# Performance work log

Measured on AMD Instinct MI355X. Metric: run time of the kernel, lower is better.

Reference implementation:

```python
import jax, jax.numpy as jnp
import numpy as np

N_NODES = 100000
N_EDGES = 1600000
IN_DIM = 128
OUT_DIM = 128


def setup_inputs() -> dict:
    key = jax.random.key(0)
    k_x, k_r, k_c, k_v, k_w, k_b = jax.random.split(key, 6)
    x = jax.random.normal(k_x, (N_NODES, IN_DIM), dtype=jnp.float32)
    rows = jax.random.randint(k_r, (N_EDGES,), 0, N_NODES, dtype=jnp.int32)
    cols = jax.random.randint(k_c, (N_EDGES,), 0, N_NODES, dtype=jnp.int32)
    vals = jax.random.uniform(k_v, (N_EDGES,), dtype=jnp.float32)
    # nn.Linear(in_dim, out_dim): kaiming-uniform-ish init, exact values irrelevant
    bound = 1.0 / np.sqrt(IN_DIM)
    W = jax.random.uniform(k_w, (IN_DIM, OUT_DIM), dtype=jnp.float32, minval=-bound, maxval=bound)
    b = jax.random.uniform(k_b, (OUT_DIM,), dtype=jnp.float32, minval=-bound, maxval=bound)
    return {"x": x, "W": W, "b": b, "vals": vals, "rows": rows, "cols": cols}


def reference(x, W, b, vals, rows, cols):
    # x = self.linear(x)
    h = x @ W + b  # [N, out_dim]
    # x = torch.sparse.mm(adj, x): out[r] += vals[e] * h[cols[e]] for each edge e with rows[e]==r
    msgs = vals[:, None] * h[cols]  # [E, out_dim]
    out = jax.ops.segment_sum(msgs, rows, num_segments=N_NODES)  # [N, out_dim]
    return out
```

## Files before the change

### kernel.cpp

```cpp
#include <hip/hip_runtime.h>

#define N_NODES 100000
#define N_EDGES 1600000
#define DIM 128
#define NBKT 1563
#define B1   256
#define EPB  6250
#define CAP2 1408
#define GEMM_NB 1563

typedef __attribute__((ext_vector_type(8))) short bf16x8;
typedef __attribute__((ext_vector_type(4))) float f32x4;

__device__ __forceinline__ unsigned short f2bf(float f) {
    unsigned u = __float_as_uint(f);
    u += 0x7FFF + ((u >> 16) & 1);
    return (unsigned short)(u >> 16);
}
__device__ __forceinline__ float bflo(unsigned u) { return __uint_as_float(u << 16); }
__device__ __forceinline__ float bfhi(unsigned u) { return __uint_as_float(u & 0xFFFF0000u); }

__global__ __launch_bounds__(256) void wt_pack(const float* __restrict__ W,
                                               uint4* __restrict__ wtf,
                                               int* __restrict__ gcnt) {
    const int t = blockIdx.x * 256 + threadIdx.x;
    if (t < NBKT) gcnt[t] = 0;
    const int f = t >> 6;
    const int l = t & 63;
    const int kc = f >> 3, nt = f & 7;
    const int quad = l >> 4, n = l & 15;
    unsigned o[4];
    #pragma unroll
    for (int jj = 0; jj < 4; ++jj) {
        const int k0 = kc * 32 + quad * 8 + jj * 2;
        const unsigned short lo = f2bf(W[(k0 + 0) * DIM + nt * 16 + n]);
        const unsigned short hi = f2bf(W[(k0 + 1) * DIM + nt * 16 + n]);
        o[jj] = (unsigned)lo | ((unsigned)hi << 16);
    }
    wtf[t] = make_uint4(o[0], o[1], o[2], o[3]);
}

#define ROWSTRIDE 136
__global__ __launch_bounds__(256) void gemm_count(const float* __restrict__ x,
                                                  const uint4* __restrict__ wtf,
                                                  const float* __restrict__ b,
                                                  unsigned short* __restrict__ h,
                                                  const int* __restrict__ rows,
                                                  int* __restrict__ gcnt) {
    __shared__ uint4 smem4[4 * 16 * ROWSTRIDE / 8];
    if (blockIdx.x >= GEMM_NB) {
        int* c = (int*)smem4;
        const int k = blockIdx.x - GEMM_NB, t = threadIdx.x;
        for (int bb = t; bb < NBKT; bb += 256) c[bb] = 0;
        __syncthreads();
        const int e0 = k * EPB;
        #pragma unroll
        for (int i = 0; i < 6; ++i) {
            const int4 r4 = *(const int4*)&rows[e0 + (t + i * 256) * 4];
            atomicAdd(&c[r4.x >> 6], 1);
            atomicAdd(&c[r4.y >> 6], 1);
            atomicAdd(&c[r4.z >> 6], 1);
            atomicAdd(&c[r4.w >> 6], 1);
        }
        if (t < EPB - 6144) atomicAdd(&c[rows[e0 + 6144 + t] >> 6], 1);
        __syncthreads();
        for (int bb = t; bb < NBKT; bb += 256) {
            const int v = c[bb];
            if (v) atomicAdd(&gcnt[bb], v);
        }
        return;
    }

    const int wave = threadIdx.x >> 6;
    const int lane = threadIdx.x & 63;
    const int quad = lane >> 4;
    const int m = lane & 15;
    const int row_base = blockIdx.x * 64 + wave * 16;
    const int row = row_base + m;
    const bool rok = (row < N_NODES);

    uint4 bf[32];
    #pragma unroll
    for (int f = 0; f < 32; ++f) bf[f] = wtf[f * 64 + lane];

    bf16x8 af[4];
    #pragma unroll
    for (int kc = 0; kc < 4; ++kc) {
        float4 v0, v1;
        if (rok) {
            v0 = *(const float4*)&x[(size_t)row * DIM + kc * 32 + quad * 8];
            v1 = *(const float4*)&x[(size_t)row * DIM + kc * 32 + quad * 8 + 4];
        } else {
            v0 = make_float4(0.f, 0.f, 0.f, 0.f);
            v1 = make_float4(0.f, 0.f, 0.f, 0.f);
        }
        union { bf16x8 v; unsigned u[4]; } a;
        a.u[0] = (unsigned)f2bf(v0.x) | ((unsigned)f2bf(v0.y) << 16);
        a.u[1] = (unsigned)f2bf(v0.z) | ((unsigned)f2bf(v0.w) << 16);
        a.u[2] = (unsigned)f2bf(v1.x) | ((unsigned)f2bf(v1.y) << 16);
        a.u[3] = (unsigned)f2bf(v1.z) | ((unsigned)f2bf(v1.w) << 16);
        af[kc] = a.v;
    }

    f32x4 acc[8];
    #pragma unroll
    for (int nt = 0; nt < 8; ++nt) {
        const float bv = b[nt * 16 + m];
        acc[nt] = (f32x4){bv, bv, bv, bv};
    }

    #pragma unroll
    for (int kc = 0; kc < 4; ++kc) {
        #pragma unroll
        for (int nt = 0; nt < 8; ++nt) {
            union { uint4 u; bf16x8 v; } bb; bb.u = bf[kc * 8 + nt];
            acc[nt] = __builtin_amdgcn_mfma_f32_16x16x32_bf16(af[kc], bb.v, acc[nt], 0, 0, 0);
        }
    }

    unsigned short* sh = (unsigned short*)smem4 + wave * 16 * ROWSTRIDE;
    #pragma unroll
    for (int nt = 0; nt < 8; ++nt) {
        #pragma unroll
        for (int i = 0; i < 4; ++i)
            sh[(quad * 4 + i) * ROWSTRIDE + nt * 16 + m] = f2bf(acc[nt][i]);
    }
    __syncthreads();
    uint4* hv4 = (uint4*)h;
    const int seg = lane & 15;
    #pragma unroll
    for (int c = 0; c < 4; ++c) {
        const int rl = (lane >> 4) + c * 4;
        const int r = row_base + rl;
        const uint4 v = *(const uint4*)&sh[rl * ROWSTRIDE + seg * 8];
        if (r < N_NODES) hv4[(size_t)r * 16 + seg] = v;
    }
}

__global__ __launch_bounds__(1024) void p1_scan(const int* __restrict__ gcnt,
                                                int* __restrict__ bktbase,
                                                int* __restrict__ gcur) {
    __shared__ int s[1024];
    const int t = threadIdx.x;
    const int i0 = 2 * t, i1 = 2 * t + 1;
    const int x0 = (i0 < NBKT) ? gcnt[i0] : 0;
    const int x1 = (i1 < NBKT) ? gcnt[i1] : 0;
    s[t] = x0 + x1;
    __syncthreads();
    for (int o = 1; o < 1024; o <<= 1) {
        const int add = (t >= o) ? s[t - o] : 0;
        __syncthreads();
        s[t] += add;
        __syncthreads();
    }
    const int excl = s[t] - x0 - x1;
    if (i0 < NBKT) { bktbase[i0] = excl; gcur[i0] = excl; }
    if (i1 <= NBKT) {
        bktbase[i1] = excl + x0;
        if (i1 < NBKT) gcur[i1] = excl + x0;
    }
}

__global__ __launch_bounds__(256) void p1_scatter(const int* __restrict__ rows,
                                                  const int* __restrict__ cols,
                                                  const float* __restrict__ vals,
                                                  int* __restrict__ gcur,
                                                  int2* __restrict__ binned) {
    __shared__ int c[NBKT];
    __shared__ int cur[NBKT];
    const int k = blockIdx.x, t = threadIdx.x;
    for (int bb = t; bb < NBKT; bb += 256) c[bb] = 0;
    __syncthreads();
    const int e0 = k * EPB;
    #pragma unroll
    for (int i = 0; i < 6; ++i) {
        const int4 r4 = *(const int4*)&rows[e0 + (t + i * 256) * 4];
        atomicAdd(&c[r4.x >> 6], 1);
        atomicAdd(&c[r4.y >> 6], 1);
        atomicAdd(&c[r4.z >> 6], 1);
        atomicAdd(&c[r4.w >> 6], 1);
    }
    if (t < EPB - 6144) atomicAdd(&c[rows[e0 + 6144 + t] >> 6], 1);
    __syncthreads();
    for (int bb = t; bb < NBKT; bb += 256) {
        const int cc = c[bb];
        if (cc) cur[bb] = atomicAdd(&gcur[bb], cc);
    }
    __syncthreads();
    #pragma unroll
    for (int i = 0; i < 6; ++i) {
        const int g = (t + i * 256) * 4;
        const int4   r4 = *(const int4*)&rows[e0 + g];
        const int4   c4 = *(const int4*)&cols[e0 + g];
        const float4 v4 = *(const float4*)&vals[e0 + g];
        int p;
        p = atomicAdd(&cur[r4.x >> 6], 1);
        binned[p] = make_int2(((r4.x & 63) << 24) | c4.x, __float_as_int(v4.x));
        p = atomicAdd(&cur[r4.y >> 6], 1);
        binned[p] = make_int2(((r4.y & 63) << 24) | c4.y, __float_as_int(v4.y));
        p = atomicAdd(&cur[r4.z >> 6], 1);
        binned[p] = make_int2(((r4.z & 63) << 24) | c4.z, __float_as_int(v4.z));
        p = atomicAdd(&cur[r4.w >> 6], 1);
        binned[p] = make_int2(((r4.w & 63) << 24) | c4.w, __float_as_int(v4.w));
    }
    if (t < EPB - 6144) {
        const int e = e0 + 6144 + t;
        const int r = rows[e];
        const int p = atomicAdd(&cur[r >> 6], 1);
        binned[p] = make_int2(((r & 63) << 24) | cols[e], __float_as_int(vals[e]));
    }
}

__global__ __launch_bounds__(256) void p2_gather(const unsigned* __restrict__ h32,
                                                 const int2* __restrict__ binned,
                                                 const int* __restrict__ bktbase,
                                                 float* __restrict__ out) {
    __shared__ int2 ebuf[CAP2];
    __shared__ int rcount[64], rstart[64], rcur[64], sscan[64];
    const int b = blockIdx.x, t = threadIdx.x;
    const int s0 = bktbase[b];
    const int n = bktbase[b + 1] - s0;

    int2 ereg[6];
    int nm = 0;
    #pragma unroll
    for (int jj = 0; jj < 6; ++jj) {
        const int j = t + jj * 256;
        if (j < n) { ereg[jj] = binned[s0 + j]; nm = jj + 1; }
    }

    if (t < 64) rcount[t] = 0;
    __syncthreads();
    #pragma unroll
    for (int jj = 0; jj < 6; ++jj)
        if (jj < nm) atomicAdd(&rcount[((unsigned)ereg[jj].x) >> 24], 1);
    __syncthreads();

    if (t < 64) sscan[t] = rcount[t];
    __syncthreads();
    for (int o = 1; o < 64; o <<= 1) {
        const int add = (t < 64 && t >= o) ? sscan[t - o] : 0;
        __syncthreads();
        if (t < 64) sscan[t] += add;
        __syncthreads();
    }
    if (t < 64) { rstart[t] = sscan[t] - rcount[t]; rcur[t] = sscan[t] - rcount[t]; }
    __syncthreads();

    #pragma unroll
    for (int jj = 0; jj < 6; ++jj)
        if (jj < nm) {
            const int lr = ((unsigned)ereg[jj].x) >> 24;
            const int pos = atomicAdd(&rcur[lr], 1);
            ebuf[pos] = make_int2(ereg[jj].x & 0x00FFFFFF, ereg[jj].y);
        }
    __syncthreads();

    const int wave = t >> 6, lane = t & 63;
    const char* hbase = (const char*)h32;
    const unsigned lane4 = (unsigned)lane * 4u;

    for (int i = 0; i < 8; ++i) {
        const int lr0 = wave * 16 + i;
        const int lr1 = lr0 + 8;
        const int r0 = b * 64 + lr0;
        const int r1 = b * 64 + lr1;
        const int st0 = rstart[lr0], cn0 = rcount[lr0];
        const int st1 = rstart[lr1], cn1 = rcount[lr1];

        float a0x = 0.f, a0y = 0.f, c0x = 0.f, c0y = 0.f;
        float a1x = 0.f, a1y = 0.f, c1x = 0.f, c1y = 0.f;
        int j0 = 0, j1 = 0;

        while (j0 + 2 <= cn0 && j1 + 2 <= cn1) {
            const int2 e0 = ebuf[st0 + j0], e1 = ebuf[st0 + j0 + 1];
            const int2 f0 = ebuf[st1 + j1], f1 = ebuf[st1 + j1 + 1];
            const unsigned u0 = *(const unsigned*)(hbase + ((((unsigned)e0.x) << 8) | lane4));
            const unsigned u1 = *(const unsigned*)(hbase + ((((unsigned)e1.x) << 8) | lane4));
            const unsigned w0 = *(const unsigned*)(hbase + ((((unsigned)f0.x) << 8) | lane4));
            const unsigned w1 = *(const unsigned*)(hbase + ((((unsigned)f1.x) << 8) | lane4));
            const float v0 = __int_as_float(e0.y), v1 = __int_as_float(e1.y);
            const float s0v = __int_as_float(f0.y), s1v = __int_as_float(f1.y);
            a0x = fmaf(v0, bflo(u0), a0x);  a0y = fmaf(v0, bfhi(u0), a0y);
            c0x = fmaf(v1, bflo(u1), c0x);  c0y = fmaf(v1, bfhi(u1), c0y);
            a1x = fmaf(s0v, bflo(w0), a1x); a1y = fmaf(s0v, bfhi(w0), a1y);
            c1x = fmaf(s1v, bflo(w1), c1x); c1y = fmaf(s1v, bfhi(w1), c1y);
            j0 += 2; j1 += 2;
        }
        for (; j0 + 2 <= cn0; j0 += 2) {
            const int2 e0 = ebuf[st0 + j0], e1 = ebuf[st0 + j0 + 1];
            const unsigned u0 = *(const unsigned*)(hbase + ((((unsigned)e0.x) << 8) | lane4));
            const unsigned u1 = *(const unsigned*)(hbase + ((((unsigned)e1.x) << 8) | lane4));
            const float v0 = __int_as_float(e0.y), v1 = __int_as_float(e1.y);
            a0x = fmaf(v0, bflo(u0), a0x); a0y = fmaf(v0, bfhi(u0), a0y);
            c0x = fmaf(v1, bflo(u1), c0x); c0y = fmaf(v1, bfhi(u1), c0y);
        }
        if (j0 < cn0) {
            const int2 e0 = ebuf[st0 + j0];
            const unsigned u0 = *(const unsigned*)(hbase + ((((unsigned)e0.x) << 8) | lane4));
            const float v0 = __int_as_float(e0.y);
            a0x = fmaf(v0, bflo(u0), a0x); a0y = fmaf(v0, bfhi(u0), a0y);
        }
        for (; j1 + 2 <= cn1; j1 += 2) {
            const int2 f0 = ebuf[st1 + j1], f1 = ebuf[st1 + j1 + 1];
            const unsigned w0 = *(const unsigned*)(hbase + ((((unsigned)f0.x) << 8) | lane4));
            const unsigned w1 = *(const unsigned*)(hbase + ((((unsigned)f1.x) << 8) | lane4));
            const float s0v = __int_as_float(f0.y), s1v = __int_as_float(f1.y);
            a1x = fmaf(s0v, bflo(w0), a1x); a1y = fmaf(s0v, bfhi(w0), a1y);
            c1x = fmaf(s1v, bflo(w1), c1x); c1y = fmaf(s1v, bfhi(w1), c1y);
        }
        if (j1 < cn1) {
            const int2 f0 = ebuf[st1 + j1];
            const unsigned w0 = *(const unsigned*)(hbase + ((((unsigned)f0.x) << 8) | lane4));
            const float s0v = __int_as_float(f0.y);
            a1x = fmaf(s0v, bflo(w0), a1x); a1y = fmaf(s0v, bfhi(w0), a1y);
        }

        if (r0 < N_NODES) {
            float2 o; o.x = a0x + c0x; o.y = a0y + c0y;
            *(float2*)&out[(size_t)r0 * DIM + lane * 2] = o;
        }
        if (r1 < N_NODES) {
            float2 o; o.x = a1x + c1x; o.y = a1y + c1y;
            *(float2*)&out[(size_t)r1 * DIM + lane * 2] = o;
        }
    }
}

extern "C" void kernel_launch(void* const* d_in, const int* in_sizes, int n_in,
                              void* d_out, int out_size, void* d_ws, size_t ws_size,
                              hipStream_t stream) {
    const float* x    = (const float*)d_in[0];
    const float* W    = (const float*)d_in[1];
    const float* b    = (const float*)d_in[2];
    const float* vals = (const float*)d_in[3];
    const int*   rows = (const int*)d_in[4];
    const int*   cols = (const int*)d_in[5];
    float* out = (float*)d_out;

    char* ws = (char*)d_ws;
    unsigned short* h = (unsigned short*)(ws + 0);
    uint4* wtf    = (uint4*)(ws + 25600000);
    int*   gcnt   = (int*)  (ws + 25632768);
    int*   bktbase= (int*)  (ws + 25639024);
    int*   gcur   = (int*)  (ws + 25645280);
    int2*  binned = (int2*) (ws + 25651536);

    wt_pack<<<8, 256, 0, stream>>>(W, wtf, gcnt);

    gemm_count<<<GEMM_NB + B1, 256, 0, stream>>>(x, wtf, b, h, rows, gcnt);

    p1_scan<<<1, 1024, 0, stream>>>(gcnt, bktbase, gcur);

    p1_scatter<<<B1, 256, 0, stream>>>(rows, cols, vals, gcur, binned);

    p2_gather<<<NBKT, 256, 0, stream>>>((const unsigned*)h, binned, bktbase, out);
}
```

Measured before the change: 229.9 us.

## Halve gather bucket size and reuse per-block histogram counts in scatter

Buckets now cover 32 rows instead of 64, giving twice as many gather blocks with 128 threads each and smaller shared edge buffers. This should improve occupancy and balance in the gather. The counting pass stores per-block bucket counts as 16-bit values, so the scatter kernel skips its own read of rows and its histogram. The in-block row scan now uses wave shuffles instead of a shared-memory loop. The trade-off is an extra workspace array and more global count writes, and the tighter CAP2 bound risks overflow if a bucket receives unusually many edges.

```diff
diff --git a/kernel.cpp b/kernel.cpp
--- a/kernel.cpp
+++ b/kernel.cpp
@@ -3,10 +3,10 @@
 #define N_NODES 100000
 #define N_EDGES 1600000
 #define DIM 128
-#define NBKT 1563
+#define NBKT 3125
 #define B1   256
 #define EPB  6250
-#define CAP2 1408
+#define CAP2 832
 #define GEMM_NB 1563
 
 typedef __attribute__((ext_vector_type(8))) short bf16x8;
@@ -24,7 +24,7 @@
                                                uint4* __restrict__ wtf,
                                                int* __restrict__ gcnt) {
     const int t = blockIdx.x * 256 + threadIdx.x;
-    if (t < NBKT) gcnt[t] = 0;
+    for (int i = t; i < NBKT; i += 2048) gcnt[i] = 0;
     const int f = t >> 6;
     const int l = t & 63;
     const int kc = f >> 3, nt = f & 7;
@@ -46,7 +46,8 @@
                                                   const float* __restrict__ b,
                                                   unsigned short* __restrict__ h,
                                                   const int* __restrict__ rows,
-                                                  int* __restrict__ gcnt) {
+                                                  int* __restrict__ gcnt,
+                                                  unsigned short* __restrict__ cnt16) {
     __shared__ uint4 smem4[4 * 16 * ROWSTRIDE / 8];
     if (blockIdx.x >= GEMM_NB) {
         int* c = (int*)smem4;
@@ -57,15 +58,16 @@
         #pragma unroll
         for (int i = 0; i < 6; ++i) {
             const int4 r4 = *(const int4*)&rows[e0 + (t + i * 256) * 4];
-            atomicAdd(&c[r4.x >> 6], 1);
-            atomicAdd(&c[r4.y >> 6], 1);
-            atomicAdd(&c[r4.z >> 6], 1);
-            atomicAdd(&c[r4.w >> 6], 1);
-        }
-        if (t < EPB - 6144) atomicAdd(&c[rows[e0 + 6144 + t] >> 6], 1);
+            atomicAdd(&c[r4.x >> 5], 1);
+            atomicAdd(&c[r4.y >> 5], 1);
+            atomicAdd(&c[r4.z >> 5], 1);
+            atomicAdd(&c[r4.w >> 5], 1);
+        }
+        if (t < EPB - 6144) atomicAdd(&c[rows[e0 + 6144 + t] >> 5], 1);
         __syncthreads();
         for (int bb = t; bb < NBKT; bb += 256) {
             const int v = c[bb];
+            cnt16[(size_t)k * NBKT + bb] = (unsigned short)v;
             if (v) atomicAdd(&gcnt[bb], v);
         }
         return;
@@ -142,10 +144,13 @@
                                                 int* __restrict__ gcur) {
     __shared__ int s[1024];
     const int t = threadIdx.x;
-    const int i0 = 2 * t, i1 = 2 * t + 1;
-    const int x0 = (i0 < NBKT) ? gcnt[i0] : 0;
-    const int x1 = (i1 < NBKT) ? gcnt[i1] : 0;
-    s[t] = x0 + x1;
+    const int base = 4 * t;
+    int x0 = (base + 0 < NBKT) ? gcnt[base + 0] : 0;
+    int x1 = (base + 1 < NBKT) ? gcnt[base + 1] : 0;
+    int x2 = (base + 2 < NBKT) ? gcnt[base + 2] : 0;
+    int x3 = (base + 3 < NBKT) ? gcnt[base + 3] : 0;
+    const int sum = x0 + x1 + x2 + x3;
+    s[t] = sum;
     __syncthreads();
     for (int o = 1; o < 1024; o <<= 1) {
         const int add = (t >= o) ? s[t - o] : 0;
@@ -153,40 +158,28 @@
         s[t] += add;
         __syncthreads();
     }
-    const int excl = s[t] - x0 - x1;
-    if (i0 < NBKT) { bktbase[i0] = excl; gcur[i0] = excl; }
-    if (i1 <= NBKT) {
-        bktbase[i1] = excl + x0;
-        if (i1 < NBKT) gcur[i1] = excl + x0;
-    }
+    int run = s[t] - sum;
+    if (base + 0 < NBKT) { bktbase[base + 0] = run; gcur[base + 0] = run; run += x0; }
+    if (base + 1 < NBKT) { bktbase[base + 1] = run; gcur[base + 1] = run; run += x1; }
+    if (base + 2 < NBKT) { bktbase[base + 2] = run; gcur[base + 2] = run; run += x2; }
+    if (base + 3 < NBKT) { bktbase[base + 3] = run; gcur[base + 3] = run; run += x3; }
+    if (base <= NBKT && NBKT < base + 4) bktbase[NBKT] = run;
 }
 
 __global__ __launch_bounds__(256) void p1_scatter(const int* __restrict__ rows,
                                                   const int* __restrict__ cols,
                                                   const float* __restrict__ vals,
+                                                  const unsigned short* __restrict__ cnt16,
                                                   int* __restrict__ gcur,
                                                   int2* __restrict__ binned) {
-    __shared__ int c[NBKT];
     __shared__ int cur[NBKT];
     const int k = blockIdx.x, t = threadIdx.x;
-    for (int bb = t; bb < NBKT; bb += 256) c[bb] = 0;
+    for (int bb = t; bb < NBKT; bb += 256) {
+        const int cc = cnt16[(size_t)k * NBKT + bb];
+        if (cc) cur[bb] = atomicAdd(&gcur[bb], cc);
+    }
     __syncthreads();
     const int e0 = k * EPB;
-    #pragma unroll
-    for (int i = 0; i < 6; ++i) {
-        const int4 r4 = *(const int4*)&rows[e0 + (t + i * 256) * 4];
-        atomicAdd(&c[r4.x >> 6], 1);
-        atomicAdd(&c[r4.y >> 6], 1);
-        atomicAdd(&c[r4.z >> 6], 1);
-        atomicAdd(&c[r4.w >> 6], 1);
-    }
-    if (t < EPB - 6144) atomicAdd(&c[rows[e0 + 6144 + t] >> 6], 1);
-    __syncthreads();
-    for (int bb = t; bb < NBKT; bb += 256) {
-        const int cc = c[bb];
-        if (cc) cur[bb] = atomicAdd(&gcur[bb], cc);
-    }
-    __syncthreads();
     #pragma unroll
     for (int i = 0; i < 6; ++i) {
         const int g = (t + i * 256) * 4;
@@ -194,61 +187,62 @@
         const int4   c4 = *(const int4*)&cols[e0 + g];
         const float4 v4 = *(const float4*)&vals[e0 + g];
         int p;
-        p = atomicAdd(&cur[r4.x >> 6], 1);
-        binned[p] = make_int2(((r4.x & 63) << 24) | c4.x, __float_as_int(v4.x));
-        p = atomicAdd(&cur[r4.y >> 6], 1);
-        binned[p] = make_int2(((r4.y & 63) << 24) | c4.y, __float_as_int(v4.y));
-        p = atomicAdd(&cur[r4.z >> 6], 1);
-        binned[p] = make_int2(((r4.z & 63) << 24) | c4.z, __float_as_int(v4.z));
-        p = atomicAdd(&cur[r4.w >> 6], 1);
-        binned[p] = make_int2(((r4.w & 63) << 24) | c4.w, __float_as_int(v4.w));
+        p = atomicAdd(&cur[r4.x >> 5], 1);
+        binned[p] = make_int2(((r4.x & 31) << 24) | c4.x, __float_as_int(v4.x));
+        p = atomicAdd(&cur[r4.y >> 5], 1);
+        binned[p] = make_int2(((r4.y & 31) << 24) | c4.y, __float_as_int(v4.y));
+        p = atomicAdd(&cur[r4.z >> 5], 1);
+        binned[p] = make_int2(((r4.z & 31) << 24) | c4.z, __float_as_int(v4.z));
+        p = atomicAdd(&cur[r4.w >> 5], 1);
+        binned[p] = make_int2(((r4.w & 31) << 24) | c4.w, __float_as_int(v4.w));
     }
     if (t < EPB - 6144) {
         const int e = e0 + 6144 + t;
         const int r = rows[e];
-        const int p = atomicAdd(&cur[r >> 6], 1);
-        binned[p] = make_int2(((r & 63) << 24) | cols[e], __float_as_int(vals[e]));
-    }
-}
-
-__global__ __launch_bounds__(256) void p2_gather(const unsigned* __restrict__ h32,
+        const int p = atomicAdd(&cur[r >> 5], 1);
+        binned[p] = make_int2(((r & 31) << 24) | cols[e], __float_as_int(vals[e]));
+    }
+}
+
+__global__ __launch_bounds__(128) void p2_gather(const unsigned* __restrict__ h32,
                                                  const int2* __restrict__ binned,
                                                  const int* __restrict__ bktbase,
                                                  float* __restrict__ out) {
     __shared__ int2 ebuf[CAP2];
-    __shared__ int rcount[64], rstart[64], rcur[64], sscan[64];
+    __shared__ int rcount[32], rstart[32], rcur[32];
     const int b = blockIdx.x, t = threadIdx.x;
     const int s0 = bktbase[b];
     const int n = bktbase[b + 1] - s0;
 
-    int2 ereg[6];
+    int2 ereg[7];
     int nm = 0;
     #pragma unroll
-    for (int jj = 0; jj < 6; ++jj) {
-        const int j = t + jj * 256;
+    for (int jj = 0; jj < 7; ++jj) {
+        const int j = t + jj * 128;
         if (j < n) { ereg[jj] = binned[s0 + j]; nm = jj + 1; }
     }
 
-    if (t < 64) rcount[t] = 0;
-    __syncthreads();
-    #pragma unroll
-    for (int jj = 0; jj < 6; ++jj)
+    if (t < 32) rcount[t] = 0;
+    __syncthreads();
+    #pragma unroll
+    for (int jj = 0; jj < 7; ++jj)
         if (jj < nm) atomicAdd(&rcount[((unsigned)ereg[jj].x) >> 24], 1);
     __syncthreads();
 
-    if (t < 64) sscan[t] = rcount[t];
-    __syncthreads();
-    for (int o = 1; o < 64; o <<= 1) {
-        const int add = (t < 64 && t >= o) ? sscan[t - o] : 0;
-        __syncthreads();
-        if (t < 64) sscan[t] += add;
-        __syncthreads();
-    }
-    if (t < 64) { rstart[t] = sscan[t] - rcount[t]; rcur[t] = sscan[t] - rcount[t]; }
-    __syncthreads();
-
-    #pragma unroll
-    for (int jj = 0; jj < 6; ++jj)
+    if (t < 64) {
+        const int c = (t < 32) ? rcount[t] : 0;
+        int v = c;
+        #pragma unroll
+        for (int o = 1; o < 32; o <<= 1) {
+            const int u = __shfl_up(v, o, 64);
+            if (t >= o) v += u;
+        }
+        if (t < 32) { rstart[t] = v - c; rcur[t] = v - c; }
+    }
+    __syncthreads();
+
+    #pragma unroll
+    for (int jj = 0; jj < 7; ++jj)
         if (jj < nm) {
             const int lr = ((unsigned)ereg[jj].x) >> 24;
             const int pos = atomicAdd(&rcur[lr], 1);
@@ -263,8 +257,8 @@
     for (int i = 0; i < 8; ++i) {
         const int lr0 = wave * 16 + i;
         const int lr1 = lr0 + 8;
-        const int r0 = b * 64 + lr0;
-        const int r1 = b * 64 + lr1;
+        const int r0 = b * 32 + lr0;
+        const int r1 = b * 32 + lr1;
         const int st0 = rstart[lr0], cn0 = rcount[lr0];
         const int st1 = rstart[lr1], cn1 = rcount[lr1];
 
@@ -316,11 +310,11 @@
             a1x = fmaf(s0v, bflo(w0), a1x); a1y = fmaf(s0v, bfhi(w0), a1y);
         }
 
-        if (r0 < N_NODES) {
+        {
             float2 o; o.x = a0x + c0x; o.y = a0y + c0y;
             *(float2*)&out[(size_t)r0 * DIM + lane * 2] = o;
         }
-        if (r1 < N_NODES) {
+        {
             float2 o; o.x = a1x + c1x; o.y = a1y + c1y;
             *(float2*)&out[(size_t)r1 * DIM + lane * 2] = o;
         }
@@ -342,17 +336,18 @@
     unsigned short* h = (unsigned short*)(ws + 0);
     uint4* wtf    = (uint4*)(ws + 25600000);
     int*   gcnt   = (int*)  (ws + 25632768);
-    int*   bktbase= (int*)  (ws + 25639024);
-    int*   gcur   = (int*)  (ws + 25645280);
-    int2*  binned = (int2*) (ws + 25651536);
+    int*   bktbase= (int*)  (ws + 25645280);
+    int*   gcur   = (int*)  (ws + 25657792);
+    unsigned short* cnt16 = (unsigned short*)(ws + 25670304);
+    int2*  binned = (int2*) (ws + 27270304);
 
     wt_pack<<<8, 256, 0, stream>>>(W, wtf, gcnt);
 
-    gemm_count<<<GEMM_NB + B1, 256, 0, stream>>>(x, wtf, b, h, rows, gcnt);
+    gemm_count<<<GEMM_NB + B1, 256, 0, stream>>>(x, wtf, b, h, rows, gcnt, cnt16);
 
     p1_scan<<<1, 1024, 0, stream>>>(gcnt, bktbase, gcur);
 
-    p1_scatter<<<B1, 256, 0, stream>>>(rows, cols, vals, gcur, binned);
-
-    p2_gather<<<NBKT, 256, 0, stream>>>((const unsigned*)h, binned, bktbase, out);
-}
+    p1_scatter<<<B1, 256, 0, stream>>>(rows, cols, vals, cnt16, gcur, binned);
+
+    p2_gather<<<NBKT, 128, 0, stream>>>((const unsigned*)h, binned, bktbase, out);
+}
```

Result: slower. 242.4 us (+5.5%).
